# Performance work log

Hardware: AMD Instinct MI355X
Metric: run time of the kernel (lower is better)

Reference implementation:

```python
import jax, jax.numpy as jnp
import numpy as np

NC = 80          # num_classes
NA = 3           # anchors per scale
G = 1.0          # offset magnitude; 1 + ceil(G/0.5) = 3
THRESH = 4.0     # anchor wh ratio threshold
BALANCE = (4.0, 1.0, 0.4)
CP, CN = 1.0, 0.0  # smooth_BCE(eps=0.0)
ANCHORS = np.array([[10, 13], [16, 30], [33, 23],
                    [30, 61], [62, 45], [59, 119],
                    [116, 90], [156, 198], [373, 326]], np.float32).reshape(3, 3, 2)
OFFS = np.array([[0, 0], [1, 0], [0, 1], [-1, 0], [0, -1]], np.float32) * G


def _build_targets(targets, grids, image_size):
    """Host-side (numpy) YOLOv7 target assignment: per-scale offset expansion,
    in-grid filtering and anchor-ratio filtering (data-dependent shapes)."""
    tcls, tbox, indices, anch = [], [], [], []
    for i, (H, W) in enumerate(grids):
        ng = np.array([H, W], np.float32)
        stride = image_size / ng                 # [sy, sx]
        anchor = ANCHORS[i] / stride[[1, 0]]     # anchors (w,h) in grid units
        gain = np.ones(6, np.float32)
        gain[2:] = (1.0 / stride)[[1, 0, 1, 0]]  # scale cx,cy,w,h to grid units
        rows = (targets * gain).reshape(-1, 6)   # [M,6]: nb,cls,cx,cy,w,h
        nb_, cls_, cx, cy, gw, gh = rows.T
        gx = cx[None, :] - OFFS[:, 0:1]          # [5,M] candidate cell x
        gy = cy[None, :] - OFFS[:, 1:2]
        brd = lambda v: np.broadcast_to(v[None, :], gx.shape)
        cand = np.stack([brd(nb_), brd(cls_), brd(cx), brd(cy),
                         gx, gy, brd(gw), brd(gh)], -1)        # [5,M,8]
        j = (gx >= 0) & (gx < ng[1]) & (gy >= 0) & (gy < ng[0])
        t = cand[j]                                             # [K,8]
        r = t[None, :, 6:8] / anchor[:, None]                   # [na,K,2]
        jj = np.maximum(r, 1.0 / r).max(-1) < THRESH            # [na,K]
        ai = np.broadcast_to(np.arange(NA, dtype=np.float32)[:, None], jj.shape)
        t = np.concatenate([np.broadcast_to(t[None], (NA,) + t.shape)[jj],
                            ai[jj][:, None]], 1)                # [n,9]
        b = t[:, 0].astype(np.int64)
        c = t[:, 1].astype(np.int64)
        gij = t[:, 4:6].astype(np.int64)                        # (gi, gj)
        a = t[:, 8].astype(np.int64)
        indices.append((jnp.asarray(b), jnp.asarray(a),
                        jnp.asarray(gij[:, 1]), jnp.asarray(gij[:, 0])))
        tbox.append(jnp.asarray(np.concatenate([t[:, 2:4] - gij, t[:, 6:8]], 1)))
        anch.append(jnp.asarray(anchor[a]))
        tcls.append(jnp.asarray(c))
    return tcls, tbox, indices, anch


def _ciou(box1, box2, eps=1e-7):
    # boxes in cxcywh, shape [n,4]
    w1, h1 = box1[:, 2], box1[:, 3]
    w2, h2 = box2[:, 2], box2[:, 3]
    b1x1, b1x2 = box1[:, 0] - w1 / 2, box1[:, 0] + w1 / 2
    b1y1, b1y2 = box1[:, 1] - h1 / 2, box1[:, 1] + h1 / 2
    b2x1, b2x2 = box2[:, 0] - w2 / 2, box2[:, 0] + w2 / 2
    b2y1, b2y2 = box2[:, 1] - h2 / 2, box2[:, 1] + h2 / 2
    inter = (jnp.clip(jnp.minimum(b1x2, b2x2) - jnp.maximum(b1x1, b2x1), 0) *
             jnp.clip(jnp.minimum(b1y2, b2y2) - jnp.maximum(b1y1, b2y1), 0))
    union = w1 * h1 + w2 * h2 - inter + eps
    iou = inter / union
    cw = jnp.maximum(b1x2, b2x2) - jnp.minimum(b1x1, b2x1)
    ch = jnp.maximum(b1y2, b2y2) - jnp.minimum(b1y1, b2y1)
    c2 = cw ** 2 + ch ** 2 + eps
    rho2 = ((b2x1 + b2x2 - b1x1 - b1x2) ** 2 +
            (b2y1 + b2y2 - b1y1 - b1y2) ** 2) / 4.0
    v = (4.0 / jnp.pi ** 2) * (jnp.arctan(w2 / (h2 + eps)) -
                               jnp.arctan(w1 / (h1 + eps))) ** 2
    alpha = jax.lax.stop_gradient(v / (v - iou + (1.0 + eps)))
    return iou - (rho2 / c2 + v * alpha)


def _bce_logits(x, t):
    # mean-reduced BCEWithLogits (pos_weight=1)
    return jnp.mean(jnp.maximum(x, 0) - x * t + jnp.log1p(jnp.exp(-jnp.abs(x))))


def _loss(preds, targets_np, image_size_np):
    grids = [p.shape[-2:] for p in preds]
    tcls, tbox, indices, anch = _build_targets(targets_np, grids, image_size_np)
    lbox = jnp.float32(0.0)
    lobj = jnp.float32(0.0)
    lcls = jnp.float32(0.0)
    for i, pi in enumerate(preds):
        B, C, H, W = pi.shape
        p = pi.reshape(B, NA, C // NA, H, W).transpose(0, 1, 3, 4, 2)  # [B,na,H,W,no]
        b, a, gj, gi = indices[i]
        tobj = jnp.zeros(p.shape[:-1], p.dtype)
        n = int(b.shape[0])
        if n:
            ps = p[b, a, gj, gi]                                       # [n,no]
            pxy = jax.nn.sigmoid(ps[:, 0:2]) * 3.0 - G                 # (1+ceil(G/0.5))=3
            pwh = (jax.nn.sigmoid(ps[:, 2:4]) * 2.0) ** 2 * anch[i]
            iou = _ciou(jnp.concatenate([pxy, pwh], 1), tbox[i])
            lbox = lbox + (1.0 - iou).mean()
            tobj = tobj.at[b, a, gj, gi].set(
                jnp.clip(jax.lax.stop_gradient(iou), 0.0).astype(p.dtype))
            if NC > 1:
                t = jnp.full((n, NC), CN, p.dtype)
                t = t.at[jnp.arange(n), tcls[i] - 1].set(CP)
                lcls = lcls + _bce_logits(ps[:, 5:], t)
        lobj = lobj + _bce_logits(p[..., 4], tobj) * BALANCE[i]
    lbox, lobj, lcls = lbox * 3.54, lobj * 64.3, lcls * 37.4
    return lbox + lobj + lcls, lbox, lobj, lcls


def setup_inputs() -> dict:
    key = jax.random.key(0)
    k0, k1, k2, k3, k4, k5 = jax.random.split(key, 6)
    B, m = 16, 12
    p0 = jax.random.normal(k0, (B, 255, 80, 80), jnp.float32)
    p1 = jax.random.normal(k1, (B, 255, 40, 40), jnp.float32)
    p2 = jax.random.normal(k2, (B, 255, 20, 20), jnp.float32)
    nb = jnp.broadcast_to(jnp.arange(B, dtype=jnp.float32)[:, None], (B, m))
    cls = jax.random.randint(k3, (B, m), 1, NC + 1).astype(jnp.float32)
    cxy = jax.random.uniform(k4, (B, m, 2), jnp.float32, 0.05, 0.95)
    wh = jax.random.uniform(k5, (B, m, 2), jnp.float32, 0.02, 0.4)
    targets = jnp.concatenate([nb[..., None], cls[..., None], cxy, wh], -1)
    image_size = jnp.array([640.0, 640.0], jnp.float32)
    return {"p0": p0, "p1": p1, "p2": p2, "targets": targets, "image_size": image_size}


def reference(p0, p1, p2, targets, image_size):
    return _loss((p0, p1, p2), np.asarray(targets), np.asarray(image_size))
```

## Files before the change

kernel.cpp:

```cpp
#include <hip/hip_runtime.h>
#include <math.h>


#define NT     192
#define NOFF   5
#define NANCH  3
#define MAXC   (NANCH*NOFF*NT)
#define THRESH 4.0f
#define NB     16
#define NCLS   80

__device__ __constant__ int   c_H[3]  = {80, 40, 20};
__device__ __constant__ int   c_W[3]  = {80, 40, 20};
__device__ __constant__ float c_anch[18] = {10,13, 16,30, 33,23,
                                            30,61, 62,45, 59,119,
                                            116,90, 156,198, 373,326};
__device__ __constant__ float c_offs[10] = {0,0, 1,0, 0,1, -1,0, 0,-1};


__device__ __forceinline__ float sigmoidf(float x) {
    return 1.0f / (1.0f + __expf(-x));
}
__device__ __forceinline__ float softplusf(float x) {
    return fmaxf(x, 0.0f) + log1pf(expf(-fabsf(x)));
}

__global__ void k_main(const float* __restrict__ p0,
                       const float* __restrict__ p1,
                       const float* __restrict__ p2,
                       const float* __restrict__ targets,
                       const float* __restrict__ image_size,
                       int* __restrict__ nctr,
                       float* __restrict__ acc) {
    const int scale = blockIdx.x;
    const int tid   = threadIdx.x;

    __shared__ float s_t[NT * 6];
    __shared__ float s_isz[2];

    if (tid == 0) {
        nctr[scale]    = 0;
        acc[4  + scale] = 0.0f;
        acc[7  + scale] = 0.0f;
        acc[10 + scale] = 0.0f;
        acc[13 + scale] = 0.0f;
        s_isz[0] = image_size[0];
        s_isz[1] = image_size[1];
    }
    for (int k = tid; k < NT * 6; k += blockDim.x) s_t[k] = targets[k];
    __syncthreads();

    const int H = c_H[scale], W = c_W[scale];
    const int HW = H * W;
    const float gx_mul = (float)W / s_isz[1];
    const float gy_mul = (float)H / s_isz[0];

    const float* p = (scale == 0) ? p0 : ((scale == 1) ? p1 : p2);

    for (int k = tid; k < MAXC; k += blockDim.x) {
        const int a   = k / (NOFF * NT);
        const int rem = k % (NOFF * NT);
        const int o   = rem / NT;
        const int t   = rem % NT;

        const float cx = s_t[t*6 + 2] * gx_mul;
        const float cy = s_t[t*6 + 3] * gy_mul;
        const float gw = s_t[t*6 + 4] * gx_mul;
        const float gh = s_t[t*6 + 5] * gy_mul;

        const float gxf = cx - c_offs[o*2 + 0];
        const float gyf = cy - c_offs[o*2 + 1];
        if (!(gxf >= 0.0f && gxf < (float)W && gyf >= 0.0f && gyf < (float)H))
            continue;

        const float aw = c_anch[(scale*3 + a)*2 + 0] * gx_mul;
        const float ah = c_anch[(scale*3 + a)*2 + 1] * gy_mul;
        const float rx = gw / aw, ry = gh / ah;
        const float mr = fmaxf(fmaxf(rx, 1.0f/rx), fmaxf(ry, 1.0f/ry));
        if (!(mr < THRESH)) continue;

        atomicAdd(&nctr[scale], 1);

        const int b   = (int)s_t[t*6 + 0];
        const int cls = (int)s_t[t*6 + 1];
        const int gi  = (int)gxf;
        const int gj  = (int)gyf;

        const float tbx = cx - (float)gi;
        const float tby = cy - (float)gj;

        const float* base = p + (size_t)b * 255 * HW + (size_t)(a * 85) * HW
                              + (size_t)gj * W + gi;

        float ps0 = base[0*HW], ps1 = base[1*(size_t)HW];
        float ps2 = base[2*(size_t)HW], ps3 = base[3*(size_t)HW];
        float ps4 = base[4*(size_t)HW];

        const float px = sigmoidf(ps0) * 3.0f - 1.0f;
        const float py = sigmoidf(ps1) * 3.0f - 1.0f;
        float pw = sigmoidf(ps2) * 2.0f; pw = pw * pw * aw;
        float ph = sigmoidf(ps3) * 2.0f; ph = ph * ph * ah;

        const float eps = 1e-7f;
        const float b1x1 = px - pw*0.5f, b1x2 = px + pw*0.5f;
        const float b1y1 = py - ph*0.5f, b1y2 = py + ph*0.5f;
        const float b2x1 = tbx - gw*0.5f, b2x2 = tbx + gw*0.5f;
        const float b2y1 = tby - gh*0.5f, b2y2 = tby + gh*0.5f;
        const float iw = fmaxf(fminf(b1x2,b2x2) - fmaxf(b1x1,b2x1), 0.0f);
        const float ih = fmaxf(fminf(b1y2,b2y2) - fmaxf(b1y1,b2y1), 0.0f);
        const float inter = iw * ih;
        const float uni   = pw*ph + gw*gh - inter + eps;
        const float iou   = inter / uni;
        const float cwid  = fmaxf(b1x2,b2x2) - fminf(b1x1,b2x1);
        const float chgt  = fmaxf(b1y2,b2y2) - fminf(b1y1,b2y1);
        const float c2    = cwid*cwid + chgt*chgt + eps;
        const float dx    = b2x1 + b2x2 - b1x1 - b1x2;
        const float dy    = b2y1 + b2y2 - b1y1 - b1y2;
        const float rho2  = (dx*dx + dy*dy) * 0.25f;
        const float dv    = atanf(gw / (gh + eps)) - atanf(pw / (ph + eps));
        const float v     = 0.4052847345693511f * dv * dv;
        const float alpha = v / (v - iou + (1.0f + eps));
        const float ciou  = iou - (rho2 / c2 + v * alpha);

        atomicAdd(&acc[10 + scale], 1.0f - ciou);
        atomicAdd(&acc[7  + scale], ps4 * fmaxf(ciou, 0.0f));

        float ls = 0.0f;
        for (int c = 0; c < NCLS; c++) {
            const float x  = base[(size_t)(5 + c) * HW];
            const float tv = (c == cls - 1) ? 1.0f : 0.0f;
            ls += fmaxf(x, 0.0f) - x * tv + log1pf(expf(-fabsf(x)));
        }
        atomicAdd(&acc[13 + scale], ls);
    }
}

__global__ void k_obj(const float* __restrict__ p0,
                      const float* __restrict__ p1,
                      const float* __restrict__ p2,
                      float* __restrict__ acc) {
    const int scale = blockIdx.y;
    const int HW = c_H[scale] * c_W[scale];
    const int N  = NB * NANCH * HW;
    const float* p = (scale == 0) ? p0 : ((scale == 1) ? p1 : p2);

    float s = 0.0f;
    const int stride = gridDim.x * blockDim.x;
    for (int i = blockIdx.x * blockDim.x + threadIdx.x; i < N; i += stride) {
        const int b   = i / (NANCH * HW);
        const int rem = i % (NANCH * HW);
        const int a   = rem / HW;
        const int pos = rem % HW;
        const float x = p[(size_t)b * 255 * HW + (size_t)(a * 85 + 4) * HW + pos];
        s += softplusf(x);
    }
    for (int off = 32; off > 0; off >>= 1) s += __shfl_down(s, off, 64);
    __shared__ float sw[4];
    const int lane = threadIdx.x & 63, wv = threadIdx.x >> 6;
    if (lane == 0) sw[wv] = s;
    __syncthreads();
    if (threadIdx.x == 0) {
        atomicAdd(&acc[4 + scale], sw[0] + sw[1] + sw[2] + sw[3]);
    }
}

__global__ void k_final(const int* __restrict__ nctr,
                        const float* __restrict__ acc,
                        float* __restrict__ out) {
    if (threadIdx.x != 0 || blockIdx.x != 0) return;
    const float bal[3] = {4.0f, 1.0f, 0.4f};
    float lobj = 0.0f, lbox = 0.0f, lcls = 0.0f;
    for (int i = 0; i < 3; i++) {
        const float cnt = (float)(NB * NANCH * c_H[i] * c_W[i]);
        lobj += (acc[4 + i] - acc[7 + i]) / cnt * bal[i];
        const int n = nctr[i];
        if (n > 0) {
            lbox += acc[10 + i] / (float)n;
            lcls += acc[13 + i] / ((float)n * (float)NCLS);
        }
    }
    lbox *= 3.54f;
    lobj *= 64.3f;
    lcls *= 37.4f;
    out[0] = lbox + lobj + lcls;
    out[1] = lbox;
    out[2] = lobj;
    out[3] = lcls;
}

extern "C" void kernel_launch(void* const* d_in, const int* in_sizes, int n_in,
                              void* d_out, int out_size, void* d_ws, size_t ws_size,
                              hipStream_t stream) {
    const float* p0  = (const float*)d_in[0];
    const float* p1  = (const float*)d_in[1];
    const float* p2  = (const float*)d_in[2];
    const float* tgt = (const float*)d_in[3];
    const float* isz = (const float*)d_in[4];
    float* out = (float*)d_out;

    int*   nctr = (int*)d_ws;
    float* acc  = (float*)d_ws;

    k_main<<<3, 256, 0, stream>>>(p0, p1, p2, tgt, isz, nctr, acc);
    k_obj<<<dim3(200, 3), 256, 0, stream>>>(p0, p1, p2, acc);
    k_final<<<1, 64, 0, stream>>>(nctr, acc, out);
}
```

Measured before the change: 160.2 us.

## Fuse target-matching, objectness and finalize into one kernel with last-block reduction

Merges the three kernels into an init kernel plus one fused kernel. In the fused kernel, 144 blocks each reduce one objectness plane with float4 loads and 3 blocks do the per-scale target matching. The last block to finish, found with an atomic counter, computes the final loss. This removes a kernel launch and the separate finalize pass and vectorises the objectness reads, but still runs the matching work in only 3 blocks.

Measured after the change: 162.3 us. Within noise of the previous version (+1.3%).

```diff
diff --git a/kernel.cpp b/kernel.cpp
--- a/kernel.cpp
+++ b/kernel.cpp
@@ -9,9 +9,12 @@
 #define THRESH 4.0f
 #define NB     16
 #define NCLS   80
+#define NPLANE 144
+#define NBLK   (NPLANE + 3)
 
 __device__ __constant__ int   c_H[3]  = {80, 40, 20};
 __device__ __constant__ int   c_W[3]  = {80, 40, 20};
+__device__ __constant__ int   c_HW[3] = {6400, 1600, 400};
 __device__ __constant__ float c_anch[18] = {10,13, 16,30, 33,23,
                                             30,61, 62,45, 59,119,
                                             116,90, 156,198, 373,326};
@@ -25,167 +28,166 @@
     return fmaxf(x, 0.0f) + log1pf(expf(-fabsf(x)));
 }
 
-__global__ void k_main(const float* __restrict__ p0,
-                       const float* __restrict__ p1,
-                       const float* __restrict__ p2,
-                       const float* __restrict__ targets,
-                       const float* __restrict__ image_size,
-                       int* __restrict__ nctr,
-                       float* __restrict__ acc) {
-    const int scale = blockIdx.x;
-    const int tid   = threadIdx.x;
-
-    __shared__ float s_t[NT * 6];
-    __shared__ float s_isz[2];
-
-    if (tid == 0) {
-        nctr[scale]    = 0;
-        acc[4  + scale] = 0.0f;
-        acc[7  + scale] = 0.0f;
-        acc[10 + scale] = 0.0f;
-        acc[13 + scale] = 0.0f;
-        s_isz[0] = image_size[0];
-        s_isz[1] = image_size[1];
-    }
-    for (int k = tid; k < NT * 6; k += blockDim.x) s_t[k] = targets[k];
-    __syncthreads();
-
-    const int H = c_H[scale], W = c_W[scale];
-    const int HW = H * W;
-    const float gx_mul = (float)W / s_isz[1];
-    const float gy_mul = (float)H / s_isz[0];
-
-    const float* p = (scale == 0) ? p0 : ((scale == 1) ? p1 : p2);
-
-    for (int k = tid; k < MAXC; k += blockDim.x) {
-        const int a   = k / (NOFF * NT);
-        const int rem = k % (NOFF * NT);
-        const int o   = rem / NT;
-        const int t   = rem % NT;
-
-        const float cx = s_t[t*6 + 2] * gx_mul;
-        const float cy = s_t[t*6 + 3] * gy_mul;
-        const float gw = s_t[t*6 + 4] * gx_mul;
-        const float gh = s_t[t*6 + 5] * gy_mul;
-
-        const float gxf = cx - c_offs[o*2 + 0];
-        const float gyf = cy - c_offs[o*2 + 1];
-        if (!(gxf >= 0.0f && gxf < (float)W && gyf >= 0.0f && gyf < (float)H))
-            continue;
-
-        const float aw = c_anch[(scale*3 + a)*2 + 0] * gx_mul;
-        const float ah = c_anch[(scale*3 + a)*2 + 1] * gy_mul;
-        const float rx = gw / aw, ry = gh / ah;
-        const float mr = fmaxf(fmaxf(rx, 1.0f/rx), fmaxf(ry, 1.0f/ry));
-        if (!(mr < THRESH)) continue;
-
-        atomicAdd(&nctr[scale], 1);
-
-        const int b   = (int)s_t[t*6 + 0];
-        const int cls = (int)s_t[t*6 + 1];
-        const int gi  = (int)gxf;
-        const int gj  = (int)gyf;
-
-        const float tbx = cx - (float)gi;
-        const float tby = cy - (float)gj;
-
-        const float* base = p + (size_t)b * 255 * HW + (size_t)(a * 85) * HW
-                              + (size_t)gj * W + gi;
-
-        float ps0 = base[0*HW], ps1 = base[1*(size_t)HW];
-        float ps2 = base[2*(size_t)HW], ps3 = base[3*(size_t)HW];
-        float ps4 = base[4*(size_t)HW];
-
-        const float px = sigmoidf(ps0) * 3.0f - 1.0f;
-        const float py = sigmoidf(ps1) * 3.0f - 1.0f;
-        float pw = sigmoidf(ps2) * 2.0f; pw = pw * pw * aw;
-        float ph = sigmoidf(ps3) * 2.0f; ph = ph * ph * ah;
-
-        const float eps = 1e-7f;
-        const float b1x1 = px - pw*0.5f, b1x2 = px + pw*0.5f;
-        const float b1y1 = py - ph*0.5f, b1y2 = py + ph*0.5f;
-        const float b2x1 = tbx - gw*0.5f, b2x2 = tbx + gw*0.5f;
-        const float b2y1 = tby - gh*0.5f, b2y2 = tby + gh*0.5f;
-        const float iw = fmaxf(fminf(b1x2,b2x2) - fmaxf(b1x1,b2x1), 0.0f);
-        const float ih = fmaxf(fminf(b1y2,b2y2) - fmaxf(b1y1,b2y1), 0.0f);
-        const float inter = iw * ih;
-        const float uni   = pw*ph + gw*gh - inter + eps;
-        const float iou   = inter / uni;
-        const float cwid  = fmaxf(b1x2,b2x2) - fminf(b1x1,b2x1);
-        const float chgt  = fmaxf(b1y2,b2y2) - fminf(b1y1,b2y1);
-        const float c2    = cwid*cwid + chgt*chgt + eps;
-        const float dx    = b2x1 + b2x2 - b1x1 - b1x2;
-        const float dy    = b2y1 + b2y2 - b1y1 - b1y2;
-        const float rho2  = (dx*dx + dy*dy) * 0.25f;
-        const float dv    = atanf(gw / (gh + eps)) - atanf(pw / (ph + eps));
-        const float v     = 0.4052847345693511f * dv * dv;
-        const float alpha = v / (v - iou + (1.0f + eps));
-        const float ciou  = iou - (rho2 / c2 + v * alpha);
-
-        atomicAdd(&acc[10 + scale], 1.0f - ciou);
-        atomicAdd(&acc[7  + scale], ps4 * fmaxf(ciou, 0.0f));
-
-        float ls = 0.0f;
-        for (int c = 0; c < NCLS; c++) {
-            const float x  = base[(size_t)(5 + c) * HW];
-            const float tv = (c == cls - 1) ? 1.0f : 0.0f;
-            ls += fmaxf(x, 0.0f) - x * tv + log1pf(expf(-fabsf(x)));
+__global__ void k_init(float* __restrict__ ws) {
+    if (threadIdx.x < 16) ws[threadIdx.x] = 0.0f;
+}
+
+__global__ void k_fused(const float* __restrict__ p0,
+                        const float* __restrict__ p1,
+                        const float* __restrict__ p2,
+                        const float* __restrict__ targets,
+                        const float* __restrict__ image_size,
+                        float* __restrict__ ws,
+                        float* __restrict__ out) {
+    const int bid = blockIdx.x;
+    const int tid = threadIdx.x;
+    int* iws = (int*)ws;
+
+    if (bid < NPLANE) {
+        const int scale = bid / (NB * NANCH);
+        const int rem   = bid % (NB * NANCH);
+        const int b     = rem / NANCH;
+        const int a     = rem % NANCH;
+        const int HW    = c_HW[scale];
+        const float* p  = (scale == 0) ? p0 : ((scale == 1) ? p1 : p2);
+        const float4* plane = (const float4*)(p + (size_t)b * 255 * HW
+                                                + (size_t)(a * 85 + 4) * HW);
+        const int n4 = HW >> 2;
+        float s = 0.0f;
+        for (int i = tid; i < n4; i += 256) {
+            const float4 v = plane[i];
+            s += softplusf(v.x) + softplusf(v.y) + softplusf(v.z) + softplusf(v.w);
         }
-        atomicAdd(&acc[13 + scale], ls);
-    }
-}
-
-__global__ void k_obj(const float* __restrict__ p0,
-                      const float* __restrict__ p1,
-                      const float* __restrict__ p2,
-                      float* __restrict__ acc) {
-    const int scale = blockIdx.y;
-    const int HW = c_H[scale] * c_W[scale];
-    const int N  = NB * NANCH * HW;
-    const float* p = (scale == 0) ? p0 : ((scale == 1) ? p1 : p2);
-
-    float s = 0.0f;
-    const int stride = gridDim.x * blockDim.x;
-    for (int i = blockIdx.x * blockDim.x + threadIdx.x; i < N; i += stride) {
-        const int b   = i / (NANCH * HW);
-        const int rem = i % (NANCH * HW);
-        const int a   = rem / HW;
-        const int pos = rem % HW;
-        const float x = p[(size_t)b * 255 * HW + (size_t)(a * 85 + 4) * HW + pos];
-        s += softplusf(x);
-    }
-    for (int off = 32; off > 0; off >>= 1) s += __shfl_down(s, off, 64);
-    __shared__ float sw[4];
-    const int lane = threadIdx.x & 63, wv = threadIdx.x >> 6;
-    if (lane == 0) sw[wv] = s;
-    __syncthreads();
-    if (threadIdx.x == 0) {
-        atomicAdd(&acc[4 + scale], sw[0] + sw[1] + sw[2] + sw[3]);
-    }
-}
-
-__global__ void k_final(const int* __restrict__ nctr,
-                        const float* __restrict__ acc,
-                        float* __restrict__ out) {
-    if (threadIdx.x != 0 || blockIdx.x != 0) return;
-    const float bal[3] = {4.0f, 1.0f, 0.4f};
-    float lobj = 0.0f, lbox = 0.0f, lcls = 0.0f;
-    for (int i = 0; i < 3; i++) {
-        const float cnt = (float)(NB * NANCH * c_H[i] * c_W[i]);
-        lobj += (acc[4 + i] - acc[7 + i]) / cnt * bal[i];
-        const int n = nctr[i];
-        if (n > 0) {
-            lbox += acc[10 + i] / (float)n;
-            lcls += acc[13 + i] / ((float)n * (float)NCLS);
+        for (int off = 32; off > 0; off >>= 1) s += __shfl_down(s, off, 64);
+        __shared__ float sw[4];
+        if ((tid & 63) == 0) sw[tid >> 6] = s;
+        __syncthreads();
+        if (tid == 0) atomicAdd(&ws[4 + scale], sw[0] + sw[1] + sw[2] + sw[3]);
+    } else {
+        const int scale = bid - NPLANE;
+        __shared__ float s_t[NT * 6];
+        __shared__ float s_isz[2];
+        if (tid == 0) { s_isz[0] = image_size[0]; s_isz[1] = image_size[1]; }
+        for (int k = tid; k < NT * 6; k += 256) s_t[k] = targets[k];
+        __syncthreads();
+
+        const int H = c_H[scale], W = c_W[scale];
+        const int HW = c_HW[scale];
+        const float gx_mul = (float)W / s_isz[1];
+        const float gy_mul = (float)H / s_isz[0];
+        const float* p = (scale == 0) ? p0 : ((scale == 1) ? p1 : p2);
+
+        for (int k = tid; k < MAXC; k += 256) {
+            const int a   = k / (NOFF * NT);
+            const int rm  = k % (NOFF * NT);
+            const int o   = rm / NT;
+            const int t   = rm % NT;
+
+            const float cx = s_t[t*6 + 2] * gx_mul;
+            const float cy = s_t[t*6 + 3] * gy_mul;
+            const float gw = s_t[t*6 + 4] * gx_mul;
+            const float gh = s_t[t*6 + 5] * gy_mul;
+
+            const float gxf = cx - c_offs[o*2 + 0];
+            const float gyf = cy - c_offs[o*2 + 1];
+            if (!(gxf >= 0.0f && gxf < (float)W && gyf >= 0.0f && gyf < (float)H))
+                continue;
+
+            const float aw = c_anch[(scale*3 + a)*2 + 0] * gx_mul;
+            const float ah = c_anch[(scale*3 + a)*2 + 1] * gy_mul;
+            const float rx = gw / aw, ry = gh / ah;
+            const float mr = fmaxf(fmaxf(rx, 1.0f/rx), fmaxf(ry, 1.0f/ry));
+            if (!(mr < THRESH)) continue;
+
+            atomicAdd(&iws[1 + scale], 1);
+
+            const int b   = (int)s_t[t*6 + 0];
+            const int cls = (int)s_t[t*6 + 1];
+            const int gi  = (int)gxf;
+            const int gj  = (int)gyf;
+            const float tbx = cx - (float)gi;
+            const float tby = cy - (float)gj;
+
+            const float* base = p + (size_t)b * 255 * HW + (size_t)(a * 85) * HW
+                                  + (size_t)gj * W + gi;
+
+            const float ps0 = base[0];
+            const float ps1 = base[(size_t)HW];
+            const float ps2 = base[2*(size_t)HW];
+            const float ps3 = base[3*(size_t)HW];
+            const float ps4 = base[4*(size_t)HW];
+
+            const float px = sigmoidf(ps0) * 3.0f - 1.0f;
+            const float py = sigmoidf(ps1) * 3.0f - 1.0f;
+            float pw = sigmoidf(ps2) * 2.0f; pw = pw * pw * aw;
+            float ph = sigmoidf(ps3) * 2.0f; ph = ph * ph * ah;
+
+            const float eps = 1e-7f;
+            const float b1x1 = px - pw*0.5f, b1x2 = px + pw*0.5f;
+            const float b1y1 = py - ph*0.5f, b1y2 = py + ph*0.5f;
+            const float b2x1 = tbx - gw*0.5f, b2x2 = tbx + gw*0.5f;
+            const float b2y1 = tby - gh*0.5f, b2y2 = tby + gh*0.5f;
+            const float iw = fmaxf(fminf(b1x2,b2x2) - fmaxf(b1x1,b2x1), 0.0f);
+            const float ih = fmaxf(fminf(b1y2,b2y2) - fmaxf(b1y1,b2y1), 0.0f);
+            const float inter = iw * ih;
+            const float uni   = pw*ph + gw*gh - inter + eps;
+            const float iou   = inter / uni;
+            const float cwid  = fmaxf(b1x2,b2x2) - fminf(b1x1,b2x1);
+            const float chgt  = fmaxf(b1y2,b2y2) - fminf(b1y1,b2y1);
+            const float c2    = cwid*cwid + chgt*chgt + eps;
+            const float dx    = b2x1 + b2x2 - b1x1 - b1x2;
+            const float dy    = b2y1 + b2y2 - b1y1 - b1y2;
+            const float rho2  = (dx*dx + dy*dy) * 0.25f;
+            const float dv    = atanf(gw / (gh + eps)) - atanf(pw / (ph + eps));
+            const float v     = 0.4052847345693511f * dv * dv;
+            const float alpha = v / (v - iou + (1.0f + eps));
+            const float ciou  = iou - (rho2 / c2 + v * alpha);
+
+            atomicAdd(&ws[10 + scale], 1.0f - ciou);
+            atomicAdd(&ws[7  + scale], ps4 * fmaxf(ciou, 0.0f));
+
+            float ls = 0.0f;
+            for (int c = 0; c < NCLS; c++) {
+                const float x  = base[(size_t)(5 + c) * HW];
+                const float tv = (c == cls - 1) ? 1.0f : 0.0f;
+                ls += fmaxf(x, 0.0f) - x * tv + log1pf(expf(-fabsf(x)));
+            }
+            atomicAdd(&ws[13 + scale], ls);
         }
     }
-    lbox *= 3.54f;
-    lobj *= 64.3f;
-    lcls *= 37.4f;
-    out[0] = lbox + lobj + lcls;
-    out[1] = lbox;
-    out[2] = lobj;
-    out[3] = lcls;
+
+    __syncthreads();
+    if (tid == 0) {
+        __threadfence();
+        const int done = atomicAdd(&iws[0], 1);
+        if (done == NBLK - 1) {
+            float a[16];
+            #pragma unroll
+            for (int i = 4; i < 16; i++) a[i] = atomicAdd(&ws[i], 0.0f);
+            int n[3];
+            #pragma unroll
+            for (int i = 0; i < 3; i++) n[i] = atomicAdd(&iws[1 + i], 0);
+
+            const float bal[3] = {4.0f, 1.0f, 0.4f};
+            float lobj = 0.0f, lbox = 0.0f, lcls = 0.0f;
+            #pragma unroll
+            for (int i = 0; i < 3; i++) {
+                const float cnt = (float)(NB * NANCH * c_HW[i]);
+                lobj += (a[4 + i] - a[7 + i]) / cnt * bal[i];
+                if (n[i] > 0) {
+                    lbox += a[10 + i] / (float)n[i];
+                    lcls += a[13 + i] / ((float)n[i] * (float)NCLS);
+                }
+            }
+            lbox *= 3.54f;
+            lobj *= 64.3f;
+            lcls *= 37.4f;
+            out[0] = lbox + lobj + lcls;
+            out[1] = lbox;
+            out[2] = lobj;
+            out[3] = lcls;
+        }
+    }
 }
 
 extern "C" void kernel_launch(void* const* d_in, const int* in_sizes, int n_in,
@@ -197,11 +199,8 @@
     const float* tgt = (const float*)d_in[3];
     const float* isz = (const float*)d_in[4];
     float* out = (float*)d_out;
-
-    int*   nctr = (int*)d_ws;
-    float* acc  = (float*)d_ws;
-
-    k_main<<<3, 256, 0, stream>>>(p0, p1, p2, tgt, isz, nctr, acc);
-    k_obj<<<dim3(200, 3), 256, 0, stream>>>(p0, p1, p2, acc);
-    k_final<<<1, 64, 0, stream>>>(nctr, acc, out);
-}
+    float* ws  = (float*)d_ws;
+
+    k_init<<<1, 64, 0, stream>>>(ws);
+    k_fused<<<NBLK, 256, 0, stream>>>(p0, p1, p2, tgt, isz, ws, out);
+}
```
